# Kernel optimization log

Measured on AMD Instinct MI355X. Metric: run time of the kernel, lower is better.

Reference implementation:

```python
import jax, jax.numpy as jnp
import numpy as np

N_NODES = 100000
N_EDGES = 1600000
D_IN = 64
D_HID = 64
N_LAYERS = 3


def setup_inputs() -> dict:
    key = jax.random.key(0)
    ks = jax.random.split(key, 10)
    inp = {
        "node_feat": jax.random.normal(ks[0], (N_NODES, D_IN), dtype=jnp.float32),
        "src": jax.random.randint(ks[1], (N_EDGES,), 0, N_NODES, dtype=jnp.int32),
        "dst": jax.random.randint(ks[2], (N_EDGES,), 0, N_NODES, dtype=jnp.int32),
        "graph_len": jnp.ones((1,), dtype=jnp.int32) * N_NODES,
    }
    # GraphConv weights: shape (in_feats, out_feats), applied as feat @ W + b (DGL xavier-style init)
    dims = [D_IN] + [D_HID] * N_LAYERS
    for i in range(N_LAYERS):
        scale = float(np.sqrt(2.0 / (dims[i] + dims[i + 1])))
        inp[f"W{i}"] = jax.random.normal(ks[3 + i], (dims[i], dims[i + 1]), dtype=jnp.float32) * scale
        inp[f"b{i}"] = jnp.zeros((dims[i + 1],), dtype=jnp.float32)
    return inp


def reference(node_feat, src, dst, graph_len, W0, b0, W1, b1, W2, b2):
    n = node_feat.shape[0]
    e = src.shape[0]
    ones = jnp.ones((e,), dtype=node_feat.dtype)
    # DGL GraphConv norm='both': src-side out-degree^{-1/2}, dst-side in-degree^{-1/2}, clamp(min=1)
    deg_out = jax.ops.segment_sum(ones, src, num_segments=n)
    deg_in = jax.ops.segment_sum(ones, dst, num_segments=n)
    inv_sqrt_out = jax.lax.rsqrt(jnp.clip(deg_out, 1.0, None))[:, None]  # [N,1]
    inv_sqrt_in = jax.lax.rsqrt(jnp.clip(deg_in, 1.0, None))[:, None]    # [N,1]

    def graph_conv(x, W, b):
        msg = (x * inv_sqrt_out)[src]                              # [E,F] gather
        agg = jax.ops.segment_sum(msg, dst, num_segments=n)        # [N,F] scatter-add
        return (agg * inv_sqrt_in) @ W + b                         # SpMM result -> dense linear

    xs = []
    h = node_feat
    for W, b in ((W0, b0), (W1, b1), (W2, b2)):
        h = jax.nn.relu(graph_conv(h, W, b))
        xs.append(h)

    # Faithful to source: torch.sum(x, dim=1) -> per-node scalar [N]; concat over layers -> [3N]
    x_pool = jnp.concatenate([x.sum(axis=1) for x in xs], axis=-1)
    xs_cat = jnp.concatenate(xs, axis=-1)  # [N, 3*H]
    return x_pool, xs_cat
```

## Files before the change

### kernel.cpp

```cpp
#include <hip/hip_runtime.h>


#define CAPB 8192
#define CAP_S2 5120
#define CPAD 16

__device__ __forceinline__ unsigned short f2bf(float f) {
  unsigned u = __float_as_uint(f);
  u += 0x7fff + ((u >> 16) & 1);
  return (unsigned short)(u >> 16);
}
__device__ __forceinline__ float bflo(unsigned u) { return __uint_as_float(u << 16); }
__device__ __forceinline__ float bfhi(unsigned u) { return __uint_as_float(u & 0xffff0000u); }

__global__ void init_zero(int* __restrict__ deg_out, int* __restrict__ cur_d, int n) {
  int t = threadIdx.x;
  int idx = blockIdx.x * 256 + t;
  if (idx < 512 * CPAD) cur_d[idx] = (idx % CPAD == 0) ? (idx / CPAD) * CAPB : 0;
  if (idx < n) deg_out[idx] = 0;
}

__global__ __launch_bounds__(1024) void scatter_both(
    const int* __restrict__ src, const int* __restrict__ dst, int e,
    int* __restrict__ cur_d, int* __restrict__ deg_out,
    unsigned* __restrict__ edges1) {
  __shared__ int hd[512];
  int t = threadIdx.x, b = blockIdx.x;
  if (t < 512) hd[t] = 0;
  __syncthreads();
  int i = b * 4096 + 4 * t;
  int sv[4], dv[4];
  if (i + 3 < e) {
    int4 s4 = *(const int4*)&src[i];
    int4 d4 = *(const int4*)&dst[i];
    sv[0] = s4.x; sv[1] = s4.y; sv[2] = s4.z; sv[3] = s4.w;
    dv[0] = d4.x; dv[1] = d4.y; dv[2] = d4.z; dv[3] = d4.w;
  } else {
    #pragma unroll
    for (int j = 0; j < 4; j++) {
      int idx = i + j;
      if (idx < e) { sv[j] = src[idx]; dv[j] = dst[idx]; }
      else { sv[j] = -1; dv[j] = -1; }
    }
  }
  #pragma unroll
  for (int k = 0; k < 4; k++) {
    if (dv[k] >= 0) {
      atomicAdd(&hd[dv[k] >> 8], 1);
      atomicAdd(&deg_out[sv[k]], 1);
    }
  }
  __syncthreads();
  if (t < 512) {
    int bd = hd[t];
    hd[t] = bd ? atomicAdd(&cur_d[t * CPAD], bd) : 0;
  }
  __syncthreads();
  #pragma unroll
  for (int k = 0; k < 4; k++) {
    if (dv[k] >= 0) {
      int pd = atomicAdd(&hd[dv[k] >> 8], 1);
      edges1[pd] = ((unsigned)sv[k] << 8) | (unsigned)(dv[k] & 255);
    }
  }
}

__global__ __launch_bounds__(512) void sort_place(
    const unsigned* __restrict__ edges1, const int* __restrict__ cur_d,
    int2* __restrict__ row_be, float* __restrict__ inv_in,
    int* __restrict__ col, int n) {
  __shared__ int sOut[CAP_S2];
  __shared__ int hist[256], cur[256], psum[256];
  int b = blockIdx.x, t = threadIdx.x;
  int sbase = b * CAPB;
  int ed = cur_d[b * CPAD];
  int rstart = b << 8;
  int nrows = min(256, n - rstart);
  if (t < 256) hist[t] = 0;
  __syncthreads();
  for (int i = sbase + t; i < ed; i += 512) atomicAdd(&hist[edges1[i] & 255u], 1);
  __syncthreads();
  int h0 = 0;
  if (t < 256) { h0 = hist[t]; psum[t] = h0; }
  __syncthreads();
  for (int off = 1; off < 256; off <<= 1) {
    int a = 0;
    if (t < 256 && t >= off) a = psum[t - off];
    __syncthreads();
    if (t < 256) psum[t] += a;
    __syncthreads();
  }
  if (t < 256) {
    int ex = psum[t] - h0;
    if (t < nrows) {
      row_be[rstart + t] = make_int2(sbase + ex, sbase + ex + h0);
      inv_in[rstart + t] = rsqrtf(fmaxf((float)h0, 1.0f));
    }
    cur[t] = ex;
  }
  __syncthreads();
  for (int i = sbase + t; i < ed; i += 512) {
    unsigned v = edges1[i];
    int pos = atomicAdd(&cur[v & 255u], 1);
    int svv = (int)(v >> 8);
    if (pos < CAP_S2) sOut[pos] = svv;
    else col[sbase + pos] = svv;
  }
  __syncthreads();
  int m = min(ed - sbase, CAP_S2);
  for (int k = t; k < m; k += 512) col[sbase + k] = sOut[k];
}

__global__ __launch_bounds__(256) void cast_xb(
    const float* __restrict__ node_feat, const int* __restrict__ deg_out,
    float* __restrict__ inv_out, unsigned short* __restrict__ xb, int n) {
  int total4 = n * 16;
  int stride = gridDim.x * 256;
  for (int u = blockIdx.x * 256 + threadIdx.x; u < total4; u += stride) {
    int r = u >> 4;
    float iv = rsqrtf(fmaxf((float)deg_out[r], 1.0f));
    if ((u & 15) == 0) inv_out[r] = iv;
    float4 v = *(const float4*)&node_feat[(size_t)u * 4];
    ushort4 o;
    o.x = f2bf(v.x * iv); o.y = f2bf(v.y * iv);
    o.z = f2bf(v.z * iv); o.w = f2bf(v.w * iv);
    *(ushort4*)&xb[(size_t)u * 4] = o;
  }
}

__global__ __launch_bounds__(512) void spmm_gemm(
    const unsigned short* __restrict__ xb,
    const int2* __restrict__ row_be,
    const int* __restrict__ col,
    const float* __restrict__ inv_in, const float* __restrict__ inv_out,
    const float* __restrict__ W, const float* __restrict__ bias,
    float* __restrict__ out_cat, float* __restrict__ out_pool,
    unsigned short* __restrict__ xb_next, int n) {
  __shared__ float sXT[64][68];
  int t = threadIdx.x;
  int row0 = blockIdx.x << 6;
  int lane = t & 63;
  int g = lane >> 3;
  int l8 = (lane & 7) << 3;
  int wv = t >> 6;
  for (int k = 0; k < 8; k++) {
    int rl = wv * 8 + k;
    int row = row0 + rl;
    float v = 0.f;
    if (row < n) {
      int2 be = row_be[row];
      int s = be.x, e = be.y;
      float inv = inv_in[row];
      float a0 = 0, a1 = 0, a2 = 0, a3 = 0, a4 = 0, a5 = 0, a6 = 0, a7 = 0;
      int ec = e - 1;
      for (int i = s + g; i < e; i += 16) {
        int i1 = i + 8;
        int c0 = col[i];
        int c1 = col[min(i1, ec)];
        float m1 = (i1 < e) ? 1.f : 0.f;
        uint4 r0 = *(const uint4*)&xb[(size_t)c0 * 64 + l8];
        uint4 r1 = *(const uint4*)&xb[(size_t)c1 * 64 + l8];
        a0 += bflo(r0.x); a1 += bfhi(r0.x); a2 += bflo(r0.y); a3 += bfhi(r0.y);
        a4 += bflo(r0.z); a5 += bfhi(r0.z); a6 += bflo(r0.w); a7 += bfhi(r0.w);
        a0 = fmaf(m1, bflo(r1.x), a0); a1 = fmaf(m1, bfhi(r1.x), a1);
        a2 = fmaf(m1, bflo(r1.y), a2); a3 = fmaf(m1, bfhi(r1.y), a3);
        a4 = fmaf(m1, bflo(r1.z), a4); a5 = fmaf(m1, bfhi(r1.z), a5);
        a6 = fmaf(m1, bflo(r1.w), a6); a7 = fmaf(m1, bfhi(r1.w), a7);
      }
      a0 += __shfl_xor(a0, 8); a0 += __shfl_xor(a0, 16); a0 += __shfl_xor(a0, 32);
      a1 += __shfl_xor(a1, 8); a1 += __shfl_xor(a1, 16); a1 += __shfl_xor(a1, 32);
      a2 += __shfl_xor(a2, 8); a2 += __shfl_xor(a2, 16); a2 += __shfl_xor(a2, 32);
      a3 += __shfl_xor(a3, 8); a3 += __shfl_xor(a3, 16); a3 += __shfl_xor(a3, 32);
      a4 += __shfl_xor(a4, 8); a4 += __shfl_xor(a4, 16); a4 += __shfl_xor(a4, 32);
      a5 += __shfl_xor(a5, 8); a5 += __shfl_xor(a5, 16); a5 += __shfl_xor(a5, 32);
      a6 += __shfl_xor(a6, 8); a6 += __shfl_xor(a6, 16); a6 += __shfl_xor(a6, 32);
      a7 += __shfl_xor(a7, 8); a7 += __shfl_xor(a7, 16); a7 += __shfl_xor(a7, 32);
      float s0 = (g & 1) ? a1 : a0;
      float s1 = (g & 1) ? a3 : a2;
      float s2 = (g & 1) ? a5 : a4;
      float s3 = (g & 1) ? a7 : a6;
      float u0 = (g & 2) ? s1 : s0;
      float u1 = (g & 2) ? s3 : s2;
      v = ((g & 4) ? u1 : u0) * inv;
    }
    sXT[l8 + g][rl] = v;
  }
  __syncthreads();
  int tj = t & 15, tr = t >> 4;
  int j4 = tj << 2, r2 = tr << 1;
  const float4 bv = *(const float4*)&bias[j4];
  float4 a0 = bv, a1 = bv;
  #pragma unroll 8
  for (int f = 0; f < 64; f++) {
    float4 w  = *(const float4*)&W[f * 64 + j4];
    float2 xv = *(const float2*)&sXT[f][r2];
    a0.x = fmaf(xv.x, w.x, a0.x); a0.y = fmaf(xv.x, w.y, a0.y);
    a0.z = fmaf(xv.x, w.z, a0.z); a0.w = fmaf(xv.x, w.w, a0.w);
    a1.x = fmaf(xv.y, w.x, a1.x); a1.y = fmaf(xv.y, w.y, a1.y);
    a1.z = fmaf(xv.y, w.z, a1.z); a1.w = fmaf(xv.y, w.w, a1.w);
  }
  float4 accs[2] = {a0, a1};
  #pragma unroll
  for (int ri = 0; ri < 2; ri++) {
    int row = row0 + r2 + ri;
    if (row < n) {
      float4 h = accs[ri];
      h.x = fmaxf(h.x, 0.f); h.y = fmaxf(h.y, 0.f);
      h.z = fmaxf(h.z, 0.f); h.w = fmaxf(h.w, 0.f);
      *(float4*)&out_cat[(size_t)row * 192 + j4] = h;
      if (xb_next) {
        float sc = inv_out[row];
        ushort4 o;
        o.x = f2bf(h.x * sc); o.y = f2bf(h.y * sc);
        o.z = f2bf(h.z * sc); o.w = f2bf(h.w * sc);
        *(ushort4*)&xb_next[(size_t)row * 64 + j4] = o;
      }
      float part = h.x + h.y + h.z + h.w;
      part += __shfl_xor(part, 1);
      part += __shfl_xor(part, 2);
      part += __shfl_xor(part, 4);
      part += __shfl_xor(part, 8);
      if (tj == 0) out_pool[row] = part;
    }
  }
}


extern "C" void kernel_launch(void* const* d_in, const int* in_sizes, int n_in,
                              void* d_out, int out_size, void* d_ws, size_t ws_size,
                              hipStream_t stream) {
  const float* node_feat = (const float*)d_in[0];
  const int* src = (const int*)d_in[1];
  const int* dst = (const int*)d_in[2];
  const float* Ws[3] = {(const float*)d_in[4], (const float*)d_in[6], (const float*)d_in[8]};
  const float* bs[3] = {(const float*)d_in[5], (const float*)d_in[7], (const float*)d_in[9]};
  float* out = (float*)d_out;
  int n = in_sizes[0] / 64;
  int e = in_sizes[1];
  int nbb = (n + 255) >> 8;
  int nblk = (e + 4095) / 4096;
  size_t slots = (size_t)nbb * CAPB;

  char* p = (char*)d_ws;
  unsigned short* xba = (unsigned short*)p; p += (size_t)n * 64 * sizeof(unsigned short);
  unsigned short* xbb = (unsigned short*)p; p += (size_t)n * 64 * sizeof(unsigned short);
  float* inv_out = (float*)p;   p += (size_t)n * sizeof(float);
  float* inv_in = (float*)p;    p += (size_t)n * sizeof(float);
  int2* row_be = (int2*)p;      p += (size_t)n * sizeof(int2);
  int* deg_out = (int*)p;       p += (size_t)n * sizeof(int);
  int* cur_d = (int*)p;         p += 512 * CPAD * sizeof(int);
  unsigned* edges1 = (unsigned*)p; p += slots * sizeof(unsigned);
  int* col = (int*)p;           p += slots * sizeof(int);

  init_zero<<<(n + 255) / 256, 256, 0, stream>>>(deg_out, cur_d, n);
  scatter_both<<<nblk, 1024, 0, stream>>>(src, dst, e, cur_d, deg_out, edges1);
  sort_place<<<nbb, 512, 0, stream>>>(edges1, cur_d, row_be, inv_in, col, n);
  cast_xb<<<1024, 256, 0, stream>>>(node_feat, deg_out, inv_out, xba, n);

  float* cat_base = out + (size_t)3 * n;
  int nfb = (n + 63) >> 6;
  spmm_gemm<<<nfb, 512, 0, stream>>>(xba, row_be, col, inv_in, inv_out,
      Ws[0], bs[0], cat_base + 0 * 64, out + (size_t)0 * n, xbb, n);
  spmm_gemm<<<nfb, 512, 0, stream>>>(xbb, row_be, col, inv_in, inv_out,
      Ws[1], bs[1], cat_base + 1 * 64, out + (size_t)1 * n, xba, n);
  spmm_gemm<<<nfb, 512, 0, stream>>>(xba, row_be, col, inv_in, inv_out,
      Ws[2], bs[2], cat_base + 2 * 64, out + (size_t)2 * n, (unsigned short*)nullptr, n);
}
```

Measured before the change: 396.8 us.

## Replace global out-degree atomics with per-block binned source scatter and local staging

Removes the per-edge global atomicAdd on deg_out and instead bins the low byte of each source by its 256-node bucket into a byte buffer. sort_place then builds the out-degree histogram in shared memory and writes inv_out. The destination scatter is also staged through shared memory with a block-local prefix sum, so global writes to edges1 become contiguous per bin. This adds extra shared-memory scans and syncs in scatter_both and an extra pass over srcbuf in sort_place.

```diff
diff --git a/kernel.cpp b/kernel.cpp
--- a/kernel.cpp
+++ b/kernel.cpp
@@ -13,72 +13,128 @@
 __device__ __forceinline__ float bflo(unsigned u) { return __uint_as_float(u << 16); }
 __device__ __forceinline__ float bfhi(unsigned u) { return __uint_as_float(u & 0xffff0000u); }
 
-__global__ void init_zero(int* __restrict__ deg_out, int* __restrict__ cur_d, int n) {
-  int t = threadIdx.x;
-  int idx = blockIdx.x * 256 + t;
-  if (idx < 512 * CPAD) cur_d[idx] = (idx % CPAD == 0) ? (idx / CPAD) * CAPB : 0;
-  if (idx < n) deg_out[idx] = 0;
+__global__ void init_zero(int* __restrict__ cur_d, int* __restrict__ cur_s) {
+  int idx = blockIdx.x * 256 + threadIdx.x;
+  if (idx < 512 * CPAD) {
+    int v = (idx % CPAD == 0) ? (idx / CPAD) * CAPB : 0;
+    cur_d[idx] = v;
+    cur_s[idx] = v;
+  }
 }
 
 __global__ __launch_bounds__(1024) void scatter_both(
     const int* __restrict__ src, const int* __restrict__ dst, int e,
-    int* __restrict__ cur_d, int* __restrict__ deg_out,
-    unsigned* __restrict__ edges1) {
-  __shared__ int hd[512];
+    int* __restrict__ cur_d, int* __restrict__ cur_s,
+    unsigned* __restrict__ edges1, unsigned char* __restrict__ srcbuf) {
+  __shared__ int stW[4096], stG[4096];
+  __shared__ int hist[512], curL[512], gofs[512], psum[512];
   int t = threadIdx.x, b = blockIdx.x;
-  if (t < 512) hd[t] = 0;
-  __syncthreads();
-  int i = b * 4096 + 4 * t;
+  int i0 = b * 4096 + 4 * t;
   int sv[4], dv[4];
-  if (i + 3 < e) {
-    int4 s4 = *(const int4*)&src[i];
-    int4 d4 = *(const int4*)&dst[i];
+  if (i0 + 3 < e) {
+    int4 s4 = *(const int4*)&src[i0];
+    int4 d4 = *(const int4*)&dst[i0];
     sv[0] = s4.x; sv[1] = s4.y; sv[2] = s4.z; sv[3] = s4.w;
     dv[0] = d4.x; dv[1] = d4.y; dv[2] = d4.z; dv[3] = d4.w;
   } else {
     #pragma unroll
     for (int j = 0; j < 4; j++) {
-      int idx = i + j;
+      int idx = i0 + j;
       if (idx < e) { sv[j] = src[idx]; dv[j] = dst[idx]; }
       else { sv[j] = -1; dv[j] = -1; }
     }
   }
+  if (t < 512) hist[t] = 0;
+  __syncthreads();
+  #pragma unroll
+  for (int k = 0; k < 4; k++)
+    if (dv[k] >= 0) atomicAdd(&hist[dv[k] >> 8], 1);
+  __syncthreads();
+  if (t < 512) psum[t] = hist[t];
+  __syncthreads();
+  for (int off = 1; off < 512; off <<= 1) {
+    int a = 0;
+    if (t < 512 && t >= off) a = psum[t - off];
+    __syncthreads();
+    if (t < 512) psum[t] += a;
+    __syncthreads();
+  }
+  if (t < 512) {
+    int cnt = hist[t];
+    int base = psum[t] - cnt;
+    curL[t] = base;
+    int g = cnt ? atomicAdd(&cur_d[t * CPAD], cnt) : 0;
+    gofs[t] = g - base;
+  }
+  __syncthreads();
   #pragma unroll
   for (int k = 0; k < 4; k++) {
     if (dv[k] >= 0) {
-      atomicAdd(&hd[dv[k] >> 8], 1);
-      atomicAdd(&deg_out[sv[k]], 1);
-    }
-  }
-  __syncthreads();
+      int bin = dv[k] >> 8;
+      int r = atomicAdd(&curL[bin], 1);
+      stW[r] = (sv[k] << 8) | (dv[k] & 255);
+      stG[r] = gofs[bin] + r;
+    }
+  }
+  __syncthreads();
+  int tot = psum[511];
+  for (int idx = t; idx < tot; idx += 1024)
+    edges1[stG[idx]] = (unsigned)stW[idx];
+  __syncthreads();
+  if (t < 512) hist[t] = 0;
+  __syncthreads();
+  #pragma unroll
+  for (int k = 0; k < 4; k++)
+    if (dv[k] >= 0) atomicAdd(&hist[sv[k] >> 8], 1);
+  __syncthreads();
+  if (t < 512) psum[t] = hist[t];
+  __syncthreads();
+  for (int off = 1; off < 512; off <<= 1) {
+    int a = 0;
+    if (t < 512 && t >= off) a = psum[t - off];
+    __syncthreads();
+    if (t < 512) psum[t] += a;
+    __syncthreads();
+  }
   if (t < 512) {
-    int bd = hd[t];
-    hd[t] = bd ? atomicAdd(&cur_d[t * CPAD], bd) : 0;
+    int cnt = hist[t];
+    int base = psum[t] - cnt;
+    curL[t] = base;
+    int g = cnt ? atomicAdd(&cur_s[t * CPAD], cnt) : 0;
+    gofs[t] = g - base;
   }
   __syncthreads();
   #pragma unroll
   for (int k = 0; k < 4; k++) {
     if (dv[k] >= 0) {
-      int pd = atomicAdd(&hd[dv[k] >> 8], 1);
-      edges1[pd] = ((unsigned)sv[k] << 8) | (unsigned)(dv[k] & 255);
-    }
-  }
+      int bin = sv[k] >> 8;
+      int r = atomicAdd(&curL[bin], 1);
+      stW[r] = sv[k] & 255;
+      stG[r] = gofs[bin] + r;
+    }
+  }
+  __syncthreads();
+  for (int idx = t; idx < tot; idx += 1024)
+    srcbuf[stG[idx]] = (unsigned char)stW[idx];
 }
 
 __global__ __launch_bounds__(512) void sort_place(
-    const unsigned* __restrict__ edges1, const int* __restrict__ cur_d,
-    int2* __restrict__ row_be, float* __restrict__ inv_in,
+    const unsigned* __restrict__ edges1, const unsigned char* __restrict__ srcbuf,
+    const int* __restrict__ cur_d, const int* __restrict__ cur_s,
+    int2* __restrict__ row_be, float* __restrict__ inv_in, float* __restrict__ inv_out,
     int* __restrict__ col, int n) {
   __shared__ int sOut[CAP_S2];
-  __shared__ int hist[256], cur[256], psum[256];
+  __shared__ int hist[256], cur[256], psum[256], dhist[256];
   int b = blockIdx.x, t = threadIdx.x;
   int sbase = b * CAPB;
   int ed = cur_d[b * CPAD];
+  int es = cur_s[b * CPAD];
   int rstart = b << 8;
   int nrows = min(256, n - rstart);
-  if (t < 256) hist[t] = 0;
+  if (t < 256) { hist[t] = 0; dhist[t] = 0; }
   __syncthreads();
   for (int i = sbase + t; i < ed; i += 512) atomicAdd(&hist[edges1[i] & 255u], 1);
+  for (int i = sbase + t; i < es; i += 512) atomicAdd(&dhist[srcbuf[i]], 1);
   __syncthreads();
   int h0 = 0;
   if (t < 256) { h0 = hist[t]; psum[t] = h0; }
@@ -95,6 +151,7 @@
     if (t < nrows) {
       row_be[rstart + t] = make_int2(sbase + ex, sbase + ex + h0);
       inv_in[rstart + t] = rsqrtf(fmaxf((float)h0, 1.0f));
+      inv_out[rstart + t] = rsqrtf(fmaxf((float)dhist[t], 1.0f));
     }
     cur[t] = ex;
   }
@@ -112,14 +169,13 @@
 }
 
 __global__ __launch_bounds__(256) void cast_xb(
-    const float* __restrict__ node_feat, const int* __restrict__ deg_out,
-    float* __restrict__ inv_out, unsigned short* __restrict__ xb, int n) {
+    const float* __restrict__ node_feat, const float* __restrict__ inv_out,
+    unsigned short* __restrict__ xb, int n) {
   int total4 = n * 16;
   int stride = gridDim.x * 256;
   for (int u = blockIdx.x * 256 + threadIdx.x; u < total4; u += stride) {
     int r = u >> 4;
-    float iv = rsqrtf(fmaxf((float)deg_out[r], 1.0f));
-    if ((u & 15) == 0) inv_out[r] = iv;
+    float iv = inv_out[r];
     float4 v = *(const float4*)&node_feat[(size_t)u * 4];
     ushort4 o;
     o.x = f2bf(v.x * iv); o.y = f2bf(v.y * iv);
@@ -247,15 +303,17 @@
   float* inv_out = (float*)p;   p += (size_t)n * sizeof(float);
   float* inv_in = (float*)p;    p += (size_t)n * sizeof(float);
   int2* row_be = (int2*)p;      p += (size_t)n * sizeof(int2);
-  int* deg_out = (int*)p;       p += (size_t)n * sizeof(int);
   int* cur_d = (int*)p;         p += 512 * CPAD * sizeof(int);
+  int* cur_s = (int*)p;         p += 512 * CPAD * sizeof(int);
   unsigned* edges1 = (unsigned*)p; p += slots * sizeof(unsigned);
   int* col = (int*)p;           p += slots * sizeof(int);
-
-  init_zero<<<(n + 255) / 256, 256, 0, stream>>>(deg_out, cur_d, n);
-  scatter_both<<<nblk, 1024, 0, stream>>>(src, dst, e, cur_d, deg_out, edges1);
-  sort_place<<<nbb, 512, 0, stream>>>(edges1, cur_d, row_be, inv_in, col, n);
-  cast_xb<<<1024, 256, 0, stream>>>(node_feat, deg_out, inv_out, xba, n);
+  unsigned char* srcbuf = (unsigned char*)p; p += slots;
+
+  init_zero<<<32, 256, 0, stream>>>(cur_d, cur_s);
+  scatter_both<<<nblk, 1024, 0, stream>>>(src, dst, e, cur_d, cur_s, edges1, srcbuf);
+  sort_place<<<nbb, 512, 0, stream>>>(edges1, srcbuf, cur_d, cur_s,
+                                      row_be, inv_in, inv_out, col, n);
+  cast_xb<<<1024, 256, 0, stream>>>(node_feat, inv_out, xba, n);
 
   float* cat_base = out + (size_t)3 * n;
   int nfb = (n + 63) >> 6;
```

Result: faster. 345.8 us (-12.9%).
